# Kernel tuning notes

Hardware: AMD Instinct MI355X
Metric: run time of the kernel (lower is better)

## Reference

```python
import jax, jax.numpy as jnp
import numpy as np

L, B, S, D, DFF, H, C = 6, 8, 2048, 1024, 4096, 16, 100
HD = D // H


def _ln(x, g, b):
    m = x.mean(-1, keepdims=True)
    v = ((x - m) ** 2).mean(-1, keepdims=True)
    return (x - m) / jnp.sqrt(v + 1e-5) * g + b


def _mha(q, k, v, wq, wk, wv, wo):
    # Faithful to source: reshape to [..., S, H, HD] WITHOUT transposing heads,
    # so matmul batches over (B, S) and scores are [..., H, H].
    def sp(t, w):
        p = t @ w
        return p.reshape(p.shape[:-1] + (H, HD))
    qh, kh, vh = sp(q, wq), sp(k, wk), sp(v, wv)
    score = jnp.matmul(qh, jnp.swapaxes(kh, -1, -2)) / np.float32(np.sqrt(HD))
    attn = jnp.matmul(jax.nn.softmax(score, axis=-1), vh)  # broadcasts leading dims
    out = attn.reshape(attn.shape[:-2] + (D,))
    return out @ wo


def setup_inputs() -> dict:
    key = jax.random.key(0)
    ks = iter(jax.random.split(key, 40))
    def n(shape, scale=0.02):
        return jax.random.normal(next(ks), shape, dtype=jnp.float32) * scale
    inp = {
        "x": jax.random.normal(next(ks), (B, S, D), dtype=jnp.float32),
        "pos": jax.random.uniform(next(ks), (1, 1, D), dtype=jnp.float32),
        "class_query": jax.random.uniform(next(ks), (1, D), dtype=jnp.float32),
    }
    for pre in ("enc", "dec"):
        for nm in ("wq", "wk", "wv", "wo"):
            inp[pre + "_" + nm] = n((L, D, D))
        inp[pre + "_w1"] = n((L, D, DFF))
        inp[pre + "_b1"] = jnp.zeros((L, DFF), jnp.float32)
        inp[pre + "_w2"] = n((L, DFF, D))
        inp[pre + "_b2"] = jnp.zeros((L, D), jnp.float32)
        for j in (1, 2):
            inp[pre + "_ln%d_g" % j] = jnp.ones((L, D), jnp.float32)
            inp[pre + "_ln%d_b" % j] = jnp.zeros((L, D), jnp.float32)
    inp["dec_ln3_g"] = jnp.ones((L, D), jnp.float32)
    inp["dec_ln3_b"] = jnp.zeros((L, D), jnp.float32)
    inp["w_out"] = n((D, C))
    inp["b_out"] = jnp.zeros((C,), jnp.float32)
    return inp


def reference(x, pos, class_query, enc_wq, enc_wk, enc_wv, enc_wo, enc_w1, enc_b1,
              enc_w2, enc_b2, enc_ln1_g, enc_ln1_b, enc_ln2_g, enc_ln2_b,
              dec_wq, dec_wk, dec_wv, dec_wo, dec_w1, dec_b1, dec_w2, dec_b2,
              dec_ln1_g, dec_ln1_b, dec_ln2_g, dec_ln2_b, dec_ln3_g, dec_ln3_b,
              w_out, b_out):
    h = x + pos
    for i in range(L):
        a = _mha(h, h, h, enc_wq[i], enc_wk[i], enc_wv[i], enc_wo[i])
        h1 = _ln(h + a, enc_ln1_g[i], enc_ln1_b[i])
        ff = jax.nn.relu(h1 @ enc_w1[i] + enc_b1[i]) @ enc_w2[i] + enc_b2[i]
        h = _ln(ff + h1, enc_ln2_g[i], enc_ln2_b[i])
    dec = class_query[None]  # [1, 1, D]
    for i in range(L):
        xd = _ln(dec + dec, dec_ln1_g[i], dec_ln1_b[i])  # eval-mode dropout(x)=x
        a = _mha(dec, h, h, dec_wq[i], dec_wk[i], dec_wv[i], dec_wo[i])
        na = _ln(xd + a, dec_ln2_g[i], dec_ln2_b[i])  # broadcasts to [B, S, D]
        ff = jax.nn.relu(na @ dec_w1[i] + dec_b1[i]) @ dec_w2[i] + dec_b2[i]
        dec = _ln(na + ff, dec_ln3_g[i], dec_ln3_b[i])
    return jnp.swapaxes(dec, 0, 1) @ w_out + b_out  # [S, B, C]
```

## Files before the change

kernel.cpp:

```cpp
#include <hip/hip_runtime.h>
#include <hip/hip_bf16.h>
#include <stdint.h>

typedef __bf16 bf16x8 __attribute__((ext_vector_type(8)));
typedef float f32x4 __attribute__((ext_vector_type(4)));
typedef unsigned short u16;
typedef u16 u16x8 __attribute__((ext_vector_type(8)));

static constexpr int TL = 6, TB = 8, TS = 2048, TD = 1024, TDFF = 4096, TC = 100;
static constexpr int TM = TB * TS;

__device__ __forceinline__ u16 f2b(float f) {
  union { float f; uint32_t u; } v; v.f = f;
  return (u16)((v.u + 0x7FFFu + ((v.u >> 16) & 1u)) >> 16);
}
__device__ __forceinline__ float b2f(u16 h) {
  union { uint32_t u; float f; } v; v.u = ((uint32_t)h) << 16;
  return v.f;
}

#define GLDS16(gp, lp) \
  __builtin_amdgcn_global_load_lds((__attribute__((address_space(1))) void*)(gp), \
                                   (__attribute__((address_space(3))) void*)(lp), 16, 0, 0)

__device__ __forceinline__ void sbar() { __builtin_amdgcn_s_barrier(); }
__device__ __forceinline__ void schedb() { __builtin_amdgcn_sched_barrier(0); }

__global__ __launch_bounds__(256) void k_addpos(const float* __restrict__ x, const float* __restrict__ pos,
                                                u16* __restrict__ hb) {
  int idx = blockIdx.x * 256 + threadIdx.x;
  float4 xv = ((const float4*)x)[idx];
  float4 pv = ((const float4*)pos)[idx & (TD / 4 - 1)];
  ushort4 ob;
  ob.x = f2b(xv.x + pv.x); ob.y = f2b(xv.y + pv.y);
  ob.z = f2b(xv.z + pv.z); ob.w = f2b(xv.w + pv.w);
  ((ushort4*)hb)[idx] = ob;
}

__global__ __launch_bounds__(256) void k_decinit(const float* __restrict__ cq, u16* __restrict__ db) {
  int idx = blockIdx.x * 256 + threadIdx.x;
  float4 v = ((const float4*)cq)[idx & (TD / 4 - 1)];
  ushort4 ob; ob.x = f2b(v.x); ob.y = f2b(v.y); ob.z = f2b(v.z); ob.w = f2b(v.w);
  ((ushort4*)db)[idx] = ob;
}

__global__ void k_tcvt(const float* __restrict__ W, u16* __restrict__ Wt, int K, int N, int Npad) {
  __shared__ float tile[32][33];
  int bn = blockIdx.x * 32, bk = blockIdx.y * 32;
  int tx = threadIdx.x, ty = threadIdx.y;
  #pragma unroll
  for (int i = ty; i < 32; i += 8) {
    int k = bk + i, n = bn + tx;
    tile[i][tx] = (k < K && n < N) ? W[(size_t)k * N + n] : 0.f;
  }
  __syncthreads();
  #pragma unroll
  for (int i = ty; i < 32; i += 8) {
    int n = bn + i, k = bk + tx;
    if (n < Npad && k < K) Wt[(size_t)n * K + k] = (n < N) ? f2b(tile[tx][i]) : (u16)0;
  }
}

template<bool HAS_BIAS>
__global__ __launch_bounds__(256) void k_ln(const u16* __restrict__ a, const u16* __restrict__ b,
                                            const float* __restrict__ bias,
                                            const float* __restrict__ g, const float* __restrict__ be,
                                            u16* __restrict__ outb) {
  int row = blockIdx.x, t = threadIdx.x;
  size_t base = (size_t)row * TD;
  ushort4 av = ((const ushort4*)(a + base))[t];
  ushort4 bv = ((const ushort4*)(b + base))[t];
  float xv[4];
  xv[0] = b2f(av.x) + b2f(bv.x);
  xv[1] = b2f(av.y) + b2f(bv.y);
  xv[2] = b2f(av.z) + b2f(bv.z);
  xv[3] = b2f(av.w) + b2f(bv.w);
  if (HAS_BIAS) {
    float4 bb = ((const float4*)bias)[t];
    xv[0] += bb.x; xv[1] += bb.y; xv[2] += bb.z; xv[3] += bb.w;
  }
  float s = xv[0] + xv[1] + xv[2] + xv[3];
  float q = xv[0] * xv[0] + xv[1] * xv[1] + xv[2] * xv[2] + xv[3] * xv[3];
  #pragma unroll
  for (int o = 32; o > 0; o >>= 1) { s += __shfl_down(s, o); q += __shfl_down(q, o); }
  __shared__ float ss[4], qs_[4];
  int wv = t >> 6;
  if ((t & 63) == 0) { ss[wv] = s; qs_[wv] = q; }
  __syncthreads();
  s = ss[0] + ss[1] + ss[2] + ss[3];
  q = qs_[0] + qs_[1] + qs_[2] + qs_[3];
  float m = s * (1.f / TD);
  float rs = rsqrtf(q * (1.f / TD) - m * m + 1e-5f);
  float4 gv = ((const float4*)g)[t];
  float4 bev = ((const float4*)be)[t];
  ushort4 ob;
  ob.x = f2b((xv[0] - m) * rs * gv.x + bev.x);
  ob.y = f2b((xv[1] - m) * rs * gv.y + bev.y);
  ob.z = f2b((xv[2] - m) * rs * gv.z + bev.z);
  ob.w = f2b((xv[3] - m) * rs * gv.w + bev.w);
  ((ushort4*)(outb + base))[t] = ob;
}

__global__ __launch_bounds__(256) void k_attn(const u16* __restrict__ Qb, const u16* __restrict__ Kb,
                                              const u16* __restrict__ Vb, u16* __restrict__ Ob) {
  constexpr int ST = 72;
  __shared__ float sh[4][3][16 * ST];
  __shared__ float ps[4][16 * 17];
  const int wv = threadIdx.x >> 6, ln = threadIdx.x & 63;
  const size_t base = ((size_t)blockIdx.x * 4 + wv) * TD;
  float* qs = sh[wv][0];
  float* ks = sh[wv][1];
  float* vs = sh[wv][2];
  #pragma unroll
  for (int it = 0; it < 4; ++it) {
    const int e = it * 256 + ln * 4;
    const int li = (e >> 6) * ST + (e & 63);
    ushort4 qv = *(const ushort4*)(Qb + base + e);
    ushort4 kv = *(const ushort4*)(Kb + base + e);
    ushort4 vv = *(const ushort4*)(Vb + base + e);
    *(float4*)(qs + li) = make_float4(b2f(qv.x), b2f(qv.y), b2f(qv.z), b2f(qv.w));
    *(float4*)(ks + li) = make_float4(b2f(kv.x), b2f(kv.y), b2f(kv.z), b2f(kv.w));
    *(float4*)(vs + li) = make_float4(b2f(vv.x), b2f(vv.y), b2f(vv.z), b2f(vv.w));
  }
  __syncthreads();
  const int hi = ln >> 2, jg = ln & 3;
  float sc[4] = {0.f, 0.f, 0.f, 0.f};
  for (int d = 0; d < 64; ++d) {
    const float qv = qs[hi * ST + d];
    #pragma unroll
    for (int jj = 0; jj < 4; ++jj) sc[jj] += qv * ks[(jg * 4 + jj) * ST + d];
  }
  #pragma unroll
  for (int jj = 0; jj < 4; ++jj) sc[jj] *= 0.125f;
  float mx = fmaxf(fmaxf(sc[0], sc[1]), fmaxf(sc[2], sc[3]));
  mx = fmaxf(mx, __shfl_xor(mx, 1, 4));
  mx = fmaxf(mx, __shfl_xor(mx, 2, 4));
  float sum = 0.f;
  #pragma unroll
  for (int jj = 0; jj < 4; ++jj) { sc[jj] = __expf(sc[jj] - mx); sum += sc[jj]; }
  sum += __shfl_xor(sum, 1, 4);
  sum += __shfl_xor(sum, 2, 4);
  const float inv = 1.f / sum;
  #pragma unroll
  for (int jj = 0; jj < 4; ++jj) ps[wv][hi * 17 + jg * 4 + jj] = sc[jj] * inv;
  __syncthreads();
  float out[16];
  #pragma unroll
  for (int t = 0; t < 16; ++t) out[t] = 0.f;
  #pragma unroll
  for (int j = 0; j < 16; ++j) {
    const float pij = ps[wv][hi * 17 + j];
    #pragma unroll
    for (int t = 0; t < 16; ++t) out[t] += pij * vs[j * ST + jg * 16 + t];
  }
  u16* op = Ob + base + hi * 64 + jg * 16;
  #pragma unroll
  for (int t4 = 0; t4 < 4; ++t4) {
    ushort4 ob;
    ob.x = f2b(out[t4 * 4 + 0]); ob.y = f2b(out[t4 * 4 + 1]);
    ob.z = f2b(out[t4 * 4 + 2]); ob.w = f2b(out[t4 * 4 + 3]);
    *(ushort4*)(op + t4 * 4) = ob;
  }
}

template<int EPI>
__global__ __launch_bounds__(512, 2) void k_gemm256(const u16* __restrict__ A, const u16* __restrict__ Bt,
                                                    u16* __restrict__ Cb, const float* __restrict__ bias,
                                                    int Nn, int Kk) {
  __shared__ __align__(16) u16 lds[67584];
  const int t = threadIdx.x;
  const int wv = t >> 6, ln = t & 63;
  const int wm = wv >> 2, wn = wv & 3;
  const int bm = blockIdx.y * 256, bn = blockIdx.x * 256;

  const int srow = t >> 3;
  const int ssc = ((t & 7) * 8) ^ ((srow & 7) << 3);
  const int fr = ln & 15;
  const int fk = (ln >> 4) * 8;
  const int fperm = (fr & 7) << 3;
  const int kc0 = fk ^ fperm;
  const int kc1 = (32 + fk) ^ fperm;
  const int arow = (wm * 128 + fr) * 64;
  const int brow = (wn * 64 + fr) * 64;

  f32x4 acc[8][4] = {};

  auto stage = [&](const u16* __restrict__ G, int half, int grow0, int kcol, int sec) {
    #pragma unroll
    for (int j = 0; j < 2; ++j) {
      const u16* gp = G + (size_t)(grow0 + half * 128 + j * 64 + srow) * Kk + kcol + ssc;
      const u16* lp = &lds[sec + half * 8192 + j * 4096 + wv * 512];
      GLDS16(gp, lp);
    }
  };

#define LA_(buf, m, ks) (*(const bf16x8*)&lds[(buf) * 32768 + arow + (m) * 1024 + ((ks) ? kc1 : kc0)])
#define LB_(buf, n, ks) (*(const bf16x8*)&lds[(buf) * 32768 + 16384 + brow + (n) * 1024 + ((ks) ? kc1 : kc0)])
#define MM_(a, b, c) __builtin_amdgcn_mfma_f32_16x16x32_bf16(a, b, c, 0, 0, 0)
#define ROW_(m, X0, X1) \
  acc[m][0] = MM_(X0, Bf00, acc[m][0]); acc[m][0] = MM_(X1, Bf01, acc[m][0]); \
  acc[m][1] = MM_(X0, Bf10, acc[m][1]); acc[m][1] = MM_(X1, Bf11, acc[m][1]); \
  acc[m][2] = MM_(X0, Bf20, acc[m][2]); acc[m][2] = MM_(X1, Bf21, acc[m][2]); \
  acc[m][3] = MM_(X0, Bf30, acc[m][3]); acc[m][3] = MM_(X1, Bf31, acc[m][3]);

  auto window = [&](int kt, int p, bool s1, bool s2, int vm) {
    const int q = p ^ 1;
    bf16x8 Bf00 = LB_(p, 0, 0), Bf01 = LB_(p, 0, 1), Bf10 = LB_(p, 1, 0), Bf11 = LB_(p, 1, 1),
           Bf20 = LB_(p, 2, 0), Bf21 = LB_(p, 2, 1), Bf30 = LB_(p, 3, 0), Bf31 = LB_(p, 3, 1);
    bf16x8 Aa0 = LA_(p, 0, 0), Aa1 = LA_(p, 0, 1), Ab0 = LA_(p, 1, 0), Ab1 = LA_(p, 1, 1);
    if (s1) stage(A, 1, bm, kt + 64, q * 32768);
    schedb(); sbar(); schedb();
    __builtin_amdgcn_s_setprio(1);
    ROW_(0, Aa0, Aa1); ROW_(1, Ab0, Ab1);
    __builtin_amdgcn_s_setprio(0);
    schedb(); sbar(); schedb();
    bf16x8 Ac0 = LA_(p, 2, 0), Ac1 = LA_(p, 2, 1), Ad0 = LA_(p, 3, 0), Ad1 = LA_(p, 3, 1);
    if (s2) stage(Bt, 0, bn, kt + 128, p * 32768 + 16384);
    schedb(); sbar(); schedb();
    __builtin_amdgcn_s_setprio(1);
    ROW_(2, Ac0, Ac1); ROW_(3, Ad0, Ad1);
    __builtin_amdgcn_s_setprio(0);
    schedb(); sbar(); schedb();
    bf16x8 Ae0 = LA_(p, 4, 0), Ae1 = LA_(p, 4, 1), Af0 = LA_(p, 5, 0), Af1 = LA_(p, 5, 1),
           Ag0 = LA_(p, 6, 0), Ag1 = LA_(p, 6, 1), Ah0 = LA_(p, 7, 0), Ah1 = LA_(p, 7, 1);
    if (s2) stage(Bt, 1, bn, kt + 128, p * 32768 + 16384);
    schedb(); sbar(); schedb();
    __builtin_amdgcn_s_setprio(1);
    ROW_(4, Ae0, Ae1); ROW_(5, Af0, Af1);
    __builtin_amdgcn_s_setprio(0);
    schedb(); sbar(); schedb();
    if (s2) stage(A, 0, bm, kt + 128, p * 32768);
    if (vm == 6)      { asm volatile("s_waitcnt vmcnt(6)" ::: "memory"); }
    else if (vm == 0) { asm volatile("s_waitcnt vmcnt(0)" ::: "memory"); }
    schedb(); sbar(); schedb();
    __builtin_amdgcn_s_setprio(1);
    ROW_(6, Ag0, Ag1); ROW_(7, Ah0, Ah1);
    __builtin_amdgcn_s_setprio(0);
    schedb(); sbar(); schedb();
  };

  stage(Bt, 0, bn, 0, 16384);
  stage(Bt, 1, bn, 0, 16384);
  stage(A,  0, bm, 0, 0);
  stage(A,  1, bm, 0, 0);
  asm volatile("s_waitcnt vmcnt(4)" ::: "memory");
  stage(Bt, 0, bn, 64, 32768 + 16384);
  stage(Bt, 1, bn, 64, 32768 + 16384);
  stage(A,  0, bm, 64, 32768);
  asm volatile("s_waitcnt vmcnt(6)" ::: "memory");
  schedb(); sbar(); schedb();

  const int nt = Kk >> 6;
  for (int tt = 0; tt < nt - 2; ++tt)
    window(tt * 64, tt & 1, true, true, 6);
  window((nt - 2) * 64, (nt - 2) & 1, true, false, 0);
  window((nt - 1) * 64, (nt - 1) & 1, false, false, -1);

  sbar();
  float bvn[4] = {0.f, 0.f, 0.f, 0.f};
  if (EPI == 1) {
    #pragma unroll
    for (int n = 0; n < 4; ++n) bvn[n] = bias[bn + wn * 64 + n * 16 + fr];
  }
  #pragma unroll
  for (int m = 0; m < 8; ++m) {
    #pragma unroll
    for (int n = 0; n < 4; ++n) {
      const int col = wn * 64 + n * 16 + fr;
      #pragma unroll
      for (int j = 0; j < 4; ++j) {
        float v = acc[m][n][j];
        if (EPI == 1) { v += bvn[n]; v = v > 0.f ? v : 0.f; }
        const int row = wm * 128 + m * 16 + (ln >> 4) * 4 + j;
        lds[row * 264 + col] = f2b(v);
      }
    }
  }
  sbar();
  #pragma unroll
  for (int it = 0; it < 16; ++it) {
    const int id = it * 512 + t;
    const int row = id >> 5, colc = (id & 31) * 8;
    u16x8 vv = *(const u16x8*)&lds[row * 264 + colc];
    *(u16x8*)&Cb[(size_t)(bm + row) * Nn + bn + colc] = vv;
  }
#undef LA_
#undef LB_
#undef MM_
#undef ROW_
}

__global__ __launch_bounds__(256) void k_gemm_out(const u16* __restrict__ A, const u16* __restrict__ Bt,
                                                  float* __restrict__ Cf, const float* __restrict__ bias,
                                                  int Nn, int Kk) {
  __shared__ __align__(16) u16 As[128 * 32];
  __shared__ __align__(16) u16 Bs[128 * 32];
  const int tid = threadIdx.x;
  const int wv = tid >> 6, ln = tid & 63;
  const int wm = wv >> 1, wn = wv & 1;
  const int bm = blockIdx.y * 128, bn = blockIdx.x * 128;
  f32x4 acc[4][4] = {};

  const int rsub = ln >> 2;
  const int koff = (ln & 3) * 8;
  const int c0 = 2 * wv, c1 = 2 * wv + 1;
  const u16* Ag0 = A + (size_t)(bm + c0 * 16 + rsub) * Kk + koff;
  const u16* Ag1 = A + (size_t)(bm + c1 * 16 + rsub) * Kk + koff;
  const u16* Bg0 = Bt + (size_t)(bn + c0 * 16 + rsub) * Kk + koff;
  const u16* Bg1 = Bt + (size_t)(bn + c1 * 16 + rsub) * Kk + koff;
  u16* As0 = &As[c0 * 512];
  u16* As1 = &As[c1 * 512];
  u16* Bs0 = &Bs[c0 * 512];
  u16* Bs1 = &Bs[c1 * 512];

  const int arow = wm * 64 + (ln & 15);
  const int brow = wn * 64 + (ln & 15);
  const int kfo = (ln >> 4) * 8;

  for (int kt = 0; kt < Kk; kt += 32) {
    GLDS16(Ag0, As0); GLDS16(Ag1, As1);
    GLDS16(Bg0, Bs0); GLDS16(Bg1, Bs1);
    Ag0 += 32; Ag1 += 32; Bg0 += 32; Bg1 += 32;
    __syncthreads();
    bf16x8 af[4], bfr[4];
    #pragma unroll
    for (int m = 0; m < 4; ++m) af[m] = *(const bf16x8*)&As[(arow + m * 16) * 32 + kfo];
    #pragma unroll
    for (int n = 0; n < 4; ++n) bfr[n] = *(const bf16x8*)&Bs[(brow + n * 16) * 32 + kfo];
    #pragma unroll
    for (int m = 0; m < 4; ++m)
      #pragma unroll
      for (int n = 0; n < 4; ++n)
        acc[m][n] = __builtin_amdgcn_mfma_f32_16x16x32_bf16(af[m], bfr[n], acc[m][n], 0, 0, 0);
    __syncthreads();
  }

  #pragma unroll
  for (int m = 0; m < 4; ++m) {
    const int row0 = bm + wm * 64 + m * 16 + (ln >> 4) * 4;
    #pragma unroll
    for (int n = 0; n < 4; ++n) {
      const int col = bn + wn * 64 + n * 16 + (ln & 15);
      #pragma unroll
      for (int j = 0; j < 4; ++j) {
        const int r = row0 + j;
        if (col < TC) {
          const int bb = r >> 11;
          const int sidx = r & (TS - 1);
          Cf[((size_t)sidx * TB + bb) * TC + col] = acc[m][n][j] + bias[col];
        }
      }
    }
  }
}

extern "C" void kernel_launch(void* const* d_in, const int* in_sizes, int n_in,
                              void* d_out, int out_size, void* d_ws, size_t ws_size,
                              hipStream_t stream) {
  (void)in_sizes; (void)n_in; (void)out_size;
  const float* x   = (const float*)d_in[0];
  const float* pos = (const float*)d_in[1];
  const float* cq  = (const float*)d_in[2];
  const float* wq_[2]   = {(const float*)d_in[3],  (const float*)d_in[15]};
  const float* wk_[2]   = {(const float*)d_in[4],  (const float*)d_in[16]};
  const float* wv_[2]   = {(const float*)d_in[5],  (const float*)d_in[17]};
  const float* wo_[2]   = {(const float*)d_in[6],  (const float*)d_in[18]};
  const float* w1_[2]   = {(const float*)d_in[7],  (const float*)d_in[19]};
  const float* b1_[2]   = {(const float*)d_in[8],  (const float*)d_in[20]};
  const float* w2_[2]   = {(const float*)d_in[9],  (const float*)d_in[21]};
  const float* b2_[2]   = {(const float*)d_in[10], (const float*)d_in[22]};
  const float* ln1g_[2] = {(const float*)d_in[11], (const float*)d_in[23]};
  const float* ln1b_[2] = {(const float*)d_in[12], (const float*)d_in[24]};
  const float* ln2g_[2] = {(const float*)d_in[13], (const float*)d_in[25]};
  const float* ln2b_[2] = {(const float*)d_in[14], (const float*)d_in[26]};
  const float* ln3g = (const float*)d_in[27];
  const float* ln3b = (const float*)d_in[28];
  const float* wout = (const float*)d_in[29];
  const float* bout = (const float*)d_in[30];

  char* ws = (char*)d_ws;
  size_t off = 0;
  auto alloc = [&](size_t bytes) {
    void* p = ws + off;
    off = (off + bytes + 255) & ~(size_t)255;
    return p;
  };
  const size_t SZ = (size_t)TM * TD * 2;
  u16* Hb   = (u16*)alloc(SZ);
  u16* DECb = (u16*)alloc(SZ);
  u16* Xb   = (u16*)alloc(SZ);
  u16* Qb   = (u16*)alloc(SZ);
  u16* Kb   = (u16*)alloc(SZ);
  u16* Vb   = (u16*)alloc(SZ);
  u16* Fb   = (u16*)alloc((size_t)TM * TDFF * 2);
  u16* WTq   = (u16*)alloc((size_t)TD * TD * 2);
  u16* WTk   = (u16*)alloc((size_t)TD * TD * 2);
  u16* WTv   = (u16*)alloc((size_t)TD * TD * 2);
  u16* WTo   = (u16*)alloc((size_t)TD * TD * 2);
  u16* WT1   = (u16*)alloc((size_t)TDFF * TD * 2);
  u16* WT2   = (u16*)alloc((size_t)TD * TDFF * 2);
  u16* WTout = (u16*)alloc((size_t)128 * TD * 2);

  if (ws_size < off) return;

  const dim3 b256(256);
  const dim3 b512(512);
  const dim3 b328(32, 8);
  const dim3 gElem(TM * TD / 4 / 256);
  const dim3 gLN(TM);
  const dim3 gAttn(TM / 4);
  const dim3 gDD(TD / 256, TM / 256);
  const dim3 gFF1(TDFF / 256, TM / 256);
  const dim3 gFF2(TD / 256, TM / 256);
  const dim3 gT_dd(TD / 32, TD / 32);
  const dim3 gT_1(TDFF / 32, TD / 32);
  const dim3 gT_2(TD / 32, TDFF / 32);

  k_addpos<<<gElem, b256, 0, stream>>>(x, pos, Hb);

  for (int p = 0; p < 2; ++p) {
    if (p == 1) k_decinit<<<gElem, b256, 0, stream>>>(cq, DECb);
    for (int i = 0; i < TL; ++i) {
      k_tcvt<<<gT_dd, b328, 0, stream>>>(wq_[p] + (size_t)i * TD * TD, WTq, TD, TD, TD);
      k_tcvt<<<gT_dd, b328, 0, stream>>>(wk_[p] + (size_t)i * TD * TD, WTk, TD, TD, TD);
      k_tcvt<<<gT_dd, b328, 0, stream>>>(wv_[p] + (size_t)i * TD * TD, WTv, TD, TD, TD);
      k_tcvt<<<gT_dd, b328, 0, stream>>>(wo_[p] + (size_t)i * TD * TD, WTo, TD, TD, TD);
      k_tcvt<<<gT_1, b328, 0, stream>>>(w1_[p] + (size_t)i * TD * TDFF, WT1, TD, TDFF, TDFF);
      k_tcvt<<<gT_2, b328, 0, stream>>>(w2_[p] + (size_t)i * TDFF * TD, WT2, TDFF, TD, TD);

      if (p == 1)
        k_ln<false><<<gLN, b256, 0, stream>>>(DECb, DECb, nullptr,
            ln1g_[1] + (size_t)i * TD, ln1b_[1] + (size_t)i * TD, Xb);

      const u16* qin = (p == 0) ? Hb : DECb;
      const u16* kvin = Hb;
      k_gemm256<0><<<gDD, b512, 0, stream>>>(qin,  WTq, Qb, nullptr, TD, TD);
      k_gemm256<0><<<gDD, b512, 0, stream>>>(kvin, WTk, Kb, nullptr, TD, TD);
      k_gemm256<0><<<gDD, b512, 0, stream>>>(kvin, WTv, Vb, nullptr, TD, TD);
      k_attn<<<gAttn, b256, 0, stream>>>(Qb, Kb, Vb, Qb);
      k_gemm256<0><<<gDD, b512, 0, stream>>>(Qb, WTo, Kb, nullptr, TD, TD);

      if (p == 0)
        k_ln<false><<<gLN, b256, 0, stream>>>(Hb, Kb, nullptr,
            ln1g_[0] + (size_t)i * TD, ln1b_[0] + (size_t)i * TD, Vb);
      else
        k_ln<false><<<gLN, b256, 0, stream>>>(Xb, Kb, nullptr,
            ln2g_[1] + (size_t)i * TD, ln2b_[1] + (size_t)i * TD, Vb);

      k_gemm256<1><<<gFF1, b512, 0, stream>>>(Vb, WT1, Fb, b1_[p] + (size_t)i * TDFF, TDFF, TD);
      k_gemm256<0><<<gFF2, b512, 0, stream>>>(Fb, WT2, Qb, nullptr, TD, TDFF);

      if (p == 0)
        k_ln<true><<<gLN, b256, 0, stream>>>(Qb, Vb, b2_[0] + (size_t)i * TD,
            ln2g_[0] + (size_t)i * TD, ln2b_[0] + (size_t)i * TD, Hb);
      else
        k_ln<true><<<gLN, b256, 0, stream>>>(Qb, Vb, b2_[1] + (size_t)i * TD,
            ln3g + (size_t)i * TD, ln3b + (size_t)i * TD, DECb);
    }
  }

  k_tcvt<<<dim3(128 / 32, TD / 32), b328, 0, stream>>>(wout, WTout, TD, TC, 128);
  k_gemm_out<<<dim3(1, TM / 128), b256, 0, stream>>>(DECb, WTout, (float*)d_out, bout, 128, TD);
}
```

Baseline: 6.399 ms.

## Fuse QKV projections into one GEMM launch and precompute staging pointers

The Q, K and V projections are now issued as one wide GEMM over the contiguous transposed weights. A new EPI==3 epilogue writes each 1024-column slice to its own output buffer. The decoder fuses only the K/V projections. Inside the GEMM, the per-stage address arithmetic is replaced by pointers that are precomputed once and bumped each step, and the K loop is unrolled by two so buffer indices become constants. This relies on the weight buffers and the Q/K/V output buffers sitting back to back in the workspace, and on the tile count along K being even.

```diff
diff --git a/kernel.cpp b/kernel.cpp
--- a/kernel.cpp
+++ b/kernel.cpp
@@ -182,18 +182,16 @@
   const int kc1 = (32 + fk) ^ fperm;
   const int arow = (wm * 128 + fr) * 64;
   const int brow = (wn * 64 + fr) * 64;
+  const int ld0 = wv * 512;
+
+  const size_t rowK = (size_t)Kk;
+  const size_t row64 = rowK * 64;
+  const u16* gA = A + (size_t)(bm + srow) * rowK + ssc;
+  const u16* gB = Bt + (size_t)(bn + srow) * rowK + ssc;
 
   f32x4 acc[8][4] = {};
 
-  auto stage = [&](const u16* __restrict__ G, int half, int grow0, int kcol, int sec) {
-    #pragma unroll
-    for (int j = 0; j < 2; ++j) {
-      const u16* gp = G + (size_t)(grow0 + half * 128 + j * 64 + srow) * Kk + kcol + ssc;
-      const u16* lp = &lds[sec + half * 8192 + j * 4096 + wv * 512];
-      GLDS16(gp, lp);
-    }
-  };
-
+#define G2_(p0, c) do { GLDS16((p0), &lds[(c) + ld0]); GLDS16((p0) + row64, &lds[(c) + 4096 + ld0]); } while (0)
 #define LA_(buf, m, ks) (*(const bf16x8*)&lds[(buf) * 32768 + arow + (m) * 1024 + ((ks) ? kc1 : kc0)])
 #define LB_(buf, n, ks) (*(const bf16x8*)&lds[(buf) * 32768 + 16384 + brow + (n) * 1024 + ((ks) ? kc1 : kc0)])
 #define MM_(a, b, c) __builtin_amdgcn_mfma_f32_16x16x32_bf16(a, b, c, 0, 0, 0)
@@ -203,58 +201,64 @@
   acc[m][2] = MM_(X0, Bf20, acc[m][2]); acc[m][2] = MM_(X1, Bf21, acc[m][2]); \
   acc[m][3] = MM_(X0, Bf30, acc[m][3]); acc[m][3] = MM_(X1, Bf31, acc[m][3]);
 
-  auto window = [&](int kt, int p, bool s1, bool s2, int vm) {
-    const int q = p ^ 1;
-    bf16x8 Bf00 = LB_(p, 0, 0), Bf01 = LB_(p, 0, 1), Bf10 = LB_(p, 1, 0), Bf11 = LB_(p, 1, 1),
-           Bf20 = LB_(p, 2, 0), Bf21 = LB_(p, 2, 1), Bf30 = LB_(p, 3, 0), Bf31 = LB_(p, 3, 1);
-    bf16x8 Aa0 = LA_(p, 0, 0), Aa1 = LA_(p, 0, 1), Ab0 = LA_(p, 1, 0), Ab1 = LA_(p, 1, 1);
-    if (s1) stage(A, 1, bm, kt + 64, q * 32768);
-    schedb(); sbar(); schedb();
-    __builtin_amdgcn_s_setprio(1);
-    ROW_(0, Aa0, Aa1); ROW_(1, Ab0, Ab1);
-    __builtin_amdgcn_s_setprio(0);
-    schedb(); sbar(); schedb();
-    bf16x8 Ac0 = LA_(p, 2, 0), Ac1 = LA_(p, 2, 1), Ad0 = LA_(p, 3, 0), Ad1 = LA_(p, 3, 1);
-    if (s2) stage(Bt, 0, bn, kt + 128, p * 32768 + 16384);
-    schedb(); sbar(); schedb();
-    __builtin_amdgcn_s_setprio(1);
-    ROW_(2, Ac0, Ac1); ROW_(3, Ad0, Ad1);
-    __builtin_amdgcn_s_setprio(0);
-    schedb(); sbar(); schedb();
-    bf16x8 Ae0 = LA_(p, 4, 0), Ae1 = LA_(p, 4, 1), Af0 = LA_(p, 5, 0), Af1 = LA_(p, 5, 1),
-           Ag0 = LA_(p, 6, 0), Ag1 = LA_(p, 6, 1), Ah0 = LA_(p, 7, 0), Ah1 = LA_(p, 7, 1);
-    if (s2) stage(Bt, 1, bn, kt + 128, p * 32768 + 16384);
-    schedb(); sbar(); schedb();
-    __builtin_amdgcn_s_setprio(1);
-    ROW_(4, Ae0, Ae1); ROW_(5, Af0, Af1);
-    __builtin_amdgcn_s_setprio(0);
-    schedb(); sbar(); schedb();
-    if (s2) stage(A, 0, bm, kt + 128, p * 32768);
-    if (vm == 6)      { asm volatile("s_waitcnt vmcnt(6)" ::: "memory"); }
-    else if (vm == 0) { asm volatile("s_waitcnt vmcnt(0)" ::: "memory"); }
-    schedb(); sbar(); schedb();
-    __builtin_amdgcn_s_setprio(1);
-    ROW_(6, Ag0, Ag1); ROW_(7, Ah0, Ah1);
-    __builtin_amdgcn_s_setprio(0);
-    schedb(); sbar(); schedb();
-  };
-
-  stage(Bt, 0, bn, 0, 16384);
-  stage(Bt, 1, bn, 0, 16384);
-  stage(A,  0, bm, 0, 0);
-  stage(A,  1, bm, 0, 0);
+#define WIN_(P, Q, S1, S2, VM) do { \
+    bf16x8 Bf00 = LB_(P,0,0), Bf01 = LB_(P,0,1), Bf10 = LB_(P,1,0), Bf11 = LB_(P,1,1), \
+           Bf20 = LB_(P,2,0), Bf21 = LB_(P,2,1), Bf30 = LB_(P,3,0), Bf31 = LB_(P,3,1); \
+    bf16x8 Aa0 = LA_(P,0,0), Aa1 = LA_(P,0,1), Ab0 = LA_(P,1,0), Ab1 = LA_(P,1,1); \
+    if (S1) { G2_(pA1, (Q) * 32768 + 8192); pA1 += 64; } \
+    schedb(); sbar(); schedb(); \
+    __builtin_amdgcn_s_setprio(1); \
+    ROW_(0, Aa0, Aa1); ROW_(1, Ab0, Ab1); \
+    __builtin_amdgcn_s_setprio(0); \
+    schedb(); sbar(); schedb(); \
+    bf16x8 Ac0 = LA_(P,2,0), Ac1 = LA_(P,2,1), Ad0 = LA_(P,3,0), Ad1 = LA_(P,3,1); \
+    if (S2) { G2_(pB0, (P) * 32768 + 16384); pB0 += 64; } \
+    schedb(); sbar(); schedb(); \
+    __builtin_amdgcn_s_setprio(1); \
+    ROW_(2, Ac0, Ac1); ROW_(3, Ad0, Ad1); \
+    __builtin_amdgcn_s_setprio(0); \
+    schedb(); sbar(); schedb(); \
+    bf16x8 Ae0 = LA_(P,4,0), Ae1 = LA_(P,4,1), Af0 = LA_(P,5,0), Af1 = LA_(P,5,1), \
+           Ag0 = LA_(P,6,0), Ag1 = LA_(P,6,1), Ah0 = LA_(P,7,0), Ah1 = LA_(P,7,1); \
+    if (S2) { G2_(pB1, (P) * 32768 + 16384 + 8192); pB1 += 64; } \
+    schedb(); sbar(); schedb(); \
+    __builtin_amdgcn_s_setprio(1); \
+    ROW_(4, Ae0, Ae1); ROW_(5, Af0, Af1); \
+    __builtin_amdgcn_s_setprio(0); \
+    schedb(); sbar(); schedb(); \
+    if (S2) { G2_(pA0, (P) * 32768); pA0 += 64; } \
+    if (VM == 6)      { asm volatile("s_waitcnt vmcnt(6)" ::: "memory"); } \
+    else if (VM == 0) { asm volatile("s_waitcnt vmcnt(0)" ::: "memory"); } \
+    schedb(); sbar(); schedb(); \
+    __builtin_amdgcn_s_setprio(1); \
+    ROW_(6, Ag0, Ag1); ROW_(7, Ah0, Ah1); \
+    __builtin_amdgcn_s_setprio(0); \
+    schedb(); sbar(); schedb(); \
+  } while (0)
+
+  G2_(gB,               16384);
+  G2_(gB + 2 * row64,   16384 + 8192);
+  G2_(gA,               0);
+  G2_(gA + 2 * row64,   8192);
   asm volatile("s_waitcnt vmcnt(4)" ::: "memory");
-  stage(Bt, 0, bn, 64, 32768 + 16384);
-  stage(Bt, 1, bn, 64, 32768 + 16384);
-  stage(A,  0, bm, 64, 32768);
+  G2_(gB + 64,              32768 + 16384);
+  G2_(gB + 2 * row64 + 64,  32768 + 16384 + 8192);
+  G2_(gA + 64,              32768);
   asm volatile("s_waitcnt vmcnt(6)" ::: "memory");
   schedb(); sbar(); schedb();
 
+  const u16* pA1 = gA + 2 * row64 + 64;
+  const u16* pB0 = gB + 128;
+  const u16* pB1 = gB + 2 * row64 + 128;
+  const u16* pA0 = gA + 128;
+
   const int nt = Kk >> 6;
-  for (int tt = 0; tt < nt - 2; ++tt)
-    window(tt * 64, tt & 1, true, true, 6);
-  window((nt - 2) * 64, (nt - 2) & 1, true, false, 0);
-  window((nt - 1) * 64, (nt - 1) & 1, false, false, -1);
+  for (int it = 0; it < (nt - 2) >> 1; ++it) {
+    WIN_(0, 1, true, true, 6);
+    WIN_(1, 0, true, true, 6);
+  }
+  WIN_(0, 1, true, false, 0);
+  WIN_(1, 0, false, false, -1);
 
   sbar();
   float bvn[4] = {0.f, 0.f, 0.f, 0.f};
@@ -277,13 +281,24 @@
     }
   }
   sbar();
+  u16* outp;
+  size_t ostride;
+  if (EPI == 3) {
+    outp = Cb + ((size_t)(bn >> 10) * TM + bm) * 1024 + (bn & 1023);
+    ostride = 1024;
+  } else {
+    outp = Cb + (size_t)bm * Nn + bn;
+    ostride = (size_t)Nn;
+  }
   #pragma unroll
   for (int it = 0; it < 16; ++it) {
     const int id = it * 512 + t;
     const int row = id >> 5, colc = (id & 31) * 8;
     u16x8 vv = *(const u16x8*)&lds[row * 264 + colc];
-    *(u16x8*)&Cb[(size_t)(bm + row) * Nn + bn + colc] = vv;
-  }
+    *(u16x8*)&outp[(size_t)row * ostride + colc] = vv;
+  }
+#undef WIN_
+#undef G2_
 #undef LA_
 #undef LB_
 #undef MM_
@@ -410,6 +425,8 @@
   const dim3 gLN(TM);
   const dim3 gAttn(TM / 4);
   const dim3 gDD(TD / 256, TM / 256);
+  const dim3 gQKV(3 * TD / 256, TM / 256);
+  const dim3 gKV(2 * TD / 256, TM / 256);
   const dim3 gFF1(TDFF / 256, TM / 256);
   const dim3 gFF2(TD / 256, TM / 256);
   const dim3 gT_dd(TD / 32, TD / 32);
@@ -432,11 +449,12 @@
         k_ln<false><<<gLN, b256, 0, stream>>>(DECb, DECb, nullptr,
             ln1g_[1] + (size_t)i * TD, ln1b_[1] + (size_t)i * TD, Xb);
 
-      const u16* qin = (p == 0) ? Hb : DECb;
-      const u16* kvin = Hb;
-      k_gemm256<0><<<gDD, b512, 0, stream>>>(qin,  WTq, Qb, nullptr, TD, TD);
-      k_gemm256<0><<<gDD, b512, 0, stream>>>(kvin, WTk, Kb, nullptr, TD, TD);
-      k_gemm256<0><<<gDD, b512, 0, stream>>>(kvin, WTv, Vb, nullptr, TD, TD);
+      if (p == 0) {
+        k_gemm256<3><<<gQKV, b512, 0, stream>>>(Hb, WTq, Qb, nullptr, 3 * TD, TD);
+      } else {
+        k_gemm256<0><<<gDD, b512, 0, stream>>>(DECb, WTq, Qb, nullptr, TD, TD);
+        k_gemm256<3><<<gKV, b512, 0, stream>>>(Hb, WTk, Kb, nullptr, 2 * TD, TD);
+      }
       k_attn<<<gAttn, b256, 0, stream>>>(Qb, Kb, Vb, Qb);
       k_gemm256<0><<<gDD, b512, 0, stream>>>(Qb, WTo, Kb, nullptr, TD, TD);
 
```

New measurement: 8.391 ms. +31.1%, slower.
